# Optimization experiments

Hardware: AMD Instinct MI355X
Metric: run time of the kernel (lower is better)

The kernel has to match this reference:

```python
import jax, jax.numpy as jnp
import numpy as np

DIM = 1024
MLP_MULT = 4
NUM_EXPERTS = 8
EXPERT_HIDDEN = MLP_MULT * DIM // NUM_EXPERTS  # 512


def setup_inputs() -> dict:
    key = jax.random.key(0)
    k_x, k_r, k_fc, k_pj = jax.random.split(key, 4)
    x = jax.random.normal(k_x, (4, 4096, DIM), dtype=jnp.float32)
    # router: nn.Linear(dim, num_experts, bias=False) -> weight [E, D]
    w_router = jax.random.normal(k_r, (NUM_EXPERTS, DIM), dtype=jnp.float32) * (1.0 / np.sqrt(DIM))
    # per-expert fc: Linear(dim, hidden) weight [H, D]; stacked [E, H, D]
    w_fc = jax.random.normal(k_fc, (NUM_EXPERTS, EXPERT_HIDDEN, DIM), dtype=jnp.float32) * (1.0 / np.sqrt(DIM))
    # per-expert proj: Linear(hidden, dim) weight [D, H]; stacked [E, D, H]
    # (_zero_init in the original; use small random values so the reference output is non-trivial)
    w_proj = jax.random.normal(k_pj, (NUM_EXPERTS, DIM, EXPERT_HIDDEN), dtype=jnp.float32) * (1.0 / np.sqrt(EXPERT_HIDDEN))
    return {"x": x, "w_router": w_router, "w_fc": w_fc, "w_proj": w_proj}


def reference(x, w_router, w_fc, w_proj):
    # Router on detached input; top-1 expert per token.
    logits = jnp.einsum('bsd,ed->bse', jax.lax.stop_gradient(x), w_router)
    weights = jax.nn.softmax(logits, axis=-1)  # computed as in original (unused in output)
    indices = jnp.argmax(weights, axis=-1)     # [B, S]
    onehot = jax.nn.one_hot(indices, NUM_EXPERTS, dtype=x.dtype)  # [B, S, E]
    # Dense dispatch: run all experts, combine with one-hot (equivalent to mask gather/scatter).
    h = jnp.einsum('bsd,ehd->bseh', x, w_fc)              # [B, S, E, H]
    h = jnp.where(h >= 0, h, 0.5 * h)                      # leaky_relu(negative_slope=0.5)
    h = h * h                                              # square
    out = jnp.einsum('bseh,edh,bse->bsd', h, w_proj, onehot)
    return out
```

## Files before the change

kernel.cpp:

```cpp
#include <hip/hip_runtime.h>
#include <stdint.h>
#include <stddef.h>

#define DIM 1024
#define NEXP 8
#define HID 512
#define NTOK 16384
#define NB_HIST 64
#define NB_ROUTER 1024
#define NB_CAST 512

typedef __attribute__((ext_vector_type(4))) float f32x4;
typedef __attribute__((ext_vector_type(8))) short short8;
typedef __attribute__((ext_vector_type(4))) unsigned short u16x4;
typedef __attribute__((ext_vector_type(8))) unsigned short u16x8;
typedef __attribute__((ext_vector_type(2))) unsigned int u32x2;
typedef __attribute__((ext_vector_type(4))) unsigned int u32x4;

__device__ __forceinline__ unsigned short f2b(float f) {
  unsigned int u = __float_as_uint(f);
  return (unsigned short)((u + 0x7FFFu + ((u >> 16) & 1u)) >> 16);
}

__device__ __forceinline__ unsigned int pk_bf16(float a, float b) {
  unsigned int r;
  asm volatile("v_cvt_pk_bf16_f32 %0, %1, %2" : "=v"(r) : "v"(a), "v"(b));
  return r;
}

__device__ __forceinline__ void gload_lds16(const unsigned short* g, unsigned short* l) {
  __builtin_amdgcn_global_load_lds((const __attribute__((address_space(1))) void*)g,
                                   (__attribute__((address_space(3))) void*)l, 16, 0, 0);
}

__global__ __launch_bounds__(256) void k_router_cast(
    const float* __restrict__ x, const float* __restrict__ wr,
    int* __restrict__ eid,
    const float* __restrict__ wfc, const float* __restrict__ wpj,
    unsigned short* __restrict__ oa, unsigned short* __restrict__ ob) {
  int bid = blockIdx.x;
  if (bid < NB_ROUTER) {
    int w = threadIdx.x >> 6, lane = threadIdx.x & 63;
    int t0 = bid * 16 + w * 4;
    const float* xr = x + (size_t)t0 * DIM;
    float s[4][NEXP];
#pragma unroll
    for (int j = 0; j < 4; j++)
#pragma unroll
      for (int e = 0; e < NEXP; e++) s[j][e] = 0.f;
#pragma unroll
    for (int i = 0; i < 4; i++) {
      f32x4 xv[4];
#pragma unroll
      for (int j = 0; j < 4; j++) xv[j] = *(const f32x4*)(xr + j * DIM + lane * 4 + 256 * i);
#pragma unroll
      for (int e = 0; e < NEXP; e++) {
        f32x4 wv = *(const f32x4*)(wr + e * DIM + lane * 4 + 256 * i);
#pragma unroll
        for (int j = 0; j < 4; j++)
          s[j][e] += xv[j].x * wv.x + xv[j].y * wv.y + xv[j].z * wv.z + xv[j].w * wv.w;
      }
    }
#pragma unroll
    for (int j = 0; j < 4; j++)
#pragma unroll
      for (int e = 0; e < NEXP; e++) {
        float v = s[j][e];
#pragma unroll
        for (int off = 32; off > 0; off >>= 1) v += __shfl_xor(v, off);
        s[j][e] = v;
      }
    if (lane == 0) {
#pragma unroll
      for (int j = 0; j < 4; j++) {
        int be = 0;
        float bv = s[j][0];
#pragma unroll
        for (int e = 1; e < NEXP; e++) {
          if (s[j][e] > bv) { bv = s[j][e]; be = e; }
        }
        eid[t0 + j] = be;
      }
    }
  } else {
    const int n4 = NEXP * HID * DIM / 4;
    int stride = NB_CAST * 256;
    for (int i = (bid - NB_ROUTER) * 256 + (int)threadIdx.x; i < n4; i += stride) {
      f32x4 va = ((const f32x4*)wfc)[i];
      f32x4 vb = ((const f32x4*)wpj)[i];
      u32x2 ua, ub;
      ua.x = pk_bf16(va.x, va.y); ua.y = pk_bf16(va.z, va.w);
      ub.x = pk_bf16(vb.x, vb.y); ub.y = pk_bf16(vb.z, vb.w);
      ((u32x2*)oa)[i] = ua;
      ((u32x2*)ob)[i] = ub;
    }
  }
}

__global__ __launch_bounds__(256) void k_hist(const int* __restrict__ eid,
                                              int* __restrict__ bc) {
  __shared__ int h[NEXP];
  if (threadIdx.x < NEXP) h[threadIdx.x] = 0;
  __syncthreads();
  int tok = blockIdx.x * (NTOK / NB_HIST) + threadIdx.x;
  atomicAdd(&h[eid[tok]], 1);
  __syncthreads();
  if (threadIdx.x < NEXP) bc[blockIdx.x * NEXP + threadIdx.x] = h[threadIdx.x];
}

__global__ void k_scan(const int* __restrict__ bc, int* __restrict__ offs,
                       int* __restrict__ base) {
  __shared__ int cnt[NEXP];
  __shared__ int so[NEXP + 1];
  int t = threadIdx.x;
  if (t < NEXP) {
    int run = 0;
    for (int b = 0; b < NB_HIST; b++) {
      base[b * NEXP + t] = run;
      run += bc[b * NEXP + t];
    }
    cnt[t] = run;
  }
  __syncthreads();
  if (t == 0) {
    int a = 0;
    for (int e = 0; e < NEXP; e++) { so[e] = a; a += cnt[e]; }
    so[NEXP] = a;
  }
  __syncthreads();
  if (t < NEXP + 1) offs[t] = so[t];
  for (int i = t; i < NB_HIST * NEXP; i += blockDim.x) base[i] += so[i % NEXP];
}

__global__ __launch_bounds__(256) void k_scatter(const int* __restrict__ eid,
                                                 const int* __restrict__ base,
                                                 int* __restrict__ tlist) {
  __shared__ int cur[NEXP];
  if (threadIdx.x < NEXP) cur[threadIdx.x] = base[blockIdx.x * NEXP + threadIdx.x];
  __syncthreads();
  int tok = blockIdx.x * (NTOK / NB_HIST) + threadIdx.x;
  int e = eid[tok];
  int pos = atomicAdd(&cur[e], 1);
  tlist[pos] = tok;
}

__device__ __forceinline__ bool tile_map(const int* offs, int NB, int& e, int& mb,
                                         int& nb) {
  int l = ((int)blockIdx.x & 7) * ((int)gridDim.x >> 3) + ((int)blockIdx.x >> 3);
  e = -1; mb = 0; nb = 0;
  int acc2 = 0;
#pragma unroll
  for (int i = 0; i < NEXP; i++) {
    int mi = offs[i + 1] - offs[i];
    int tb = ((mi + 127) >> 7) * NB;
    if (e < 0 && l < acc2 + tb) {
      int r = l - acc2;
      e = i; mb = r / NB; nb = r % NB;
    }
    acc2 += tb;
  }
  return e >= 0;
}

__global__ __launch_bounds__(256) void k_gemm_fc(
    const float* __restrict__ x, const unsigned short* __restrict__ wb,
    const int* __restrict__ offs, const int* __restrict__ tlist,
    unsigned short* __restrict__ hout) {
  constexpr int KDIM = DIM, NDIM = HID;
  int e, mb, nb;
  if (!tile_map(offs, 4, e, mb, nb)) return;
  int off = offs[e], me = offs[e + 1] - off, m0 = mb * 128, n0 = nb * 128;

  __shared__ unsigned short As[3][128 * 32];
  __shared__ unsigned short Bs[3][128 * 32];

  int t = threadIdx.x, lane = t & 63, w = t >> 6;
  int wm = w >> 1, wn = w & 1;

  int kb = (lane & 3) ^ ((lane >> 3) & 3);

  const unsigned short* bsrc[2];
  const float* af32[2];
#pragma unroll
  for (int i = 0; i < 2; i++) {
    int r = i * 64 + w * 16 + (lane >> 2);
    bsrc[i] = wb + ((size_t)e * NDIM + n0 + r) * (size_t)KDIM + kb * 8;
    int gm = m0 + r;
    if (gm > me - 1) gm = me - 1;
    af32[i] = x + (size_t)tlist[off + gm] * DIM + kb * 8;
  }
  int awoff0 = (w * 16) * 32 + lane * 8;
  int awoff1 = (64 + w * 16) * 32 + lane * 8;

  f32x4 acc[4][4] = {};
  constexpr int NT = KDIM / 32;

  unsigned short* a0 = &As[0][0]; unsigned short* b0 = &Bs[0][0];
  unsigned short* a1 = &As[1][0]; unsigned short* b1 = &Bs[1][0];
  unsigned short* a2 = &As[2][0]; unsigned short* b2 = &Bs[2][0];

  f32x4 r00, r01, r10, r11;

#define ISSUE_A(kt_)                                              \
  do {                                                            \
    r00 = *(const f32x4*)(af32[0] + (kt_) * 32);                  \
    r01 = *(const f32x4*)(af32[0] + (kt_) * 32 + 4);              \
    r10 = *(const f32x4*)(af32[1] + (kt_) * 32);                  \
    r11 = *(const f32x4*)(af32[1] + (kt_) * 32 + 4);              \
  } while (0)
#define ISSUE_B(kt_, db_)                                         \
  do {                                                            \
    gload_lds16(bsrc[0] + (kt_) * 32, (db_) + (w * 16) * 32);     \
    gload_lds16(bsrc[1] + (kt_) * 32, (db_) + (64 + w * 16) * 32);\
  } while (0)
#define WRITE_A(da_)                                              \
  do {                                                            \
    u32x4 c0, c1;                                                 \
    c0.x = pk_bf16(r00.x, r00.y); c0.y = pk_bf16(r00.z, r00.w);   \
    c0.z = pk_bf16(r01.x, r01.y); c0.w = pk_bf16(r01.z, r01.w);   \
    c1.x = pk_bf16(r10.x, r10.y); c1.y = pk_bf16(r10.z, r10.w);   \
    c1.z = pk_bf16(r11.x, r11.y); c1.w = pk_bf16(r11.z, r11.w);   \
    *(u32x4*)&(da_)[awoff0] = c0;                                 \
    *(u32x4*)&(da_)[awoff1] = c1;                                 \
  } while (0)

  ISSUE_A(0);
  ISSUE_B(0, b0);
  ISSUE_B(1, b1);

  for (int kt = 0; kt < NT; kt++) {
    if (kt == NT - 1) {
      asm volatile("s_waitcnt vmcnt(0)" ::: "memory");
    } else {
      asm volatile("s_waitcnt vmcnt(2)" ::: "memory");
    }
    __builtin_amdgcn_sched_barrier(0);
    WRITE_A(a0);
    asm volatile("s_waitcnt lgkmcnt(0)" ::: "memory");
    __builtin_amdgcn_sched_barrier(0);
    __builtin_amdgcn_s_barrier();
    if (kt + 1 < NT) ISSUE_A(kt + 1);
    if (kt + 2 < NT) ISSUE_B(kt + 2, b2);

    short8 af[4], bf[4];
#pragma unroll
    for (int i = 0; i < 4; i++) {
      int ra = wm * 64 + i * 16 + (lane & 15);
      int ca = (lane >> 4) ^ ((ra >> 1) & 3);
      af[i] = *(const short8*)&a0[ra * 32 + ca * 8];
      int rbb = wn * 64 + i * 16 + (lane & 15);
      int cb = (lane >> 4) ^ ((rbb >> 1) & 3);
      bf[i] = *(const short8*)&b0[rbb * 32 + cb * 8];
    }
    __builtin_amdgcn_s_setprio(1);
#pragma unroll
    for (int mi = 0; mi < 4; mi++)
#pragma unroll
      for (int ni = 0; ni < 4; ni++)
        acc[mi][ni] =
            __builtin_amdgcn_mfma_f32_16x16x32_bf16(af[mi], bf[ni], acc[mi][ni], 0, 0, 0);
    __builtin_amdgcn_s_setprio(0);

    unsigned short* ta = a0; a0 = a1; a1 = a2; a2 = ta;
    unsigned short* tb = b0; b0 = b1; b1 = b2; b2 = tb;
  }
#undef ISSUE_A
#undef ISSUE_B
#undef WRITE_A

  int rb = (lane >> 4) * 4, cb = lane & 15;
#pragma unroll
  for (int mi = 0; mi < 4; mi++) {
#pragma unroll
    for (int j = 0; j < 4; j++) {
      int ml = wm * 64 + mi * 16 + rb + j;
      if (m0 + ml < me) {
#pragma unroll
        for (int ni = 0; ni < 4; ni++) {
          int col = n0 + wn * 64 + ni * 16 + cb;
          float v = acc[mi][ni][j];
          v = (v >= 0.f) ? v * v : 0.25f * v * v;
          hout[(size_t)(off + m0 + ml) * HID + col] = f2b(v);
        }
      }
    }
  }
}

__global__ __launch_bounds__(256) void k_gemm_pj(
    const unsigned short* __restrict__ hin, const unsigned short* __restrict__ wb,
    const int* __restrict__ offs, const int* __restrict__ tlist,
    float* __restrict__ out) {
  constexpr int KDIM = HID, NDIM = DIM;
  int e, mb, nb;
  if (!tile_map(offs, 8, e, mb, nb)) return;
  int off = offs[e], me = offs[e + 1] - off, m0 = mb * 128, n0 = nb * 128;

  __shared__ unsigned short lds[3][2][128 * 32];

  int t = threadIdx.x, lane = t & 63, w = t >> 6;
  int wm = w >> 1, wn = w & 1;

  int kb = (lane & 3) ^ ((lane >> 3) & 3);

  const unsigned short* asrc[2];
  const unsigned short* bsrc[2];
#pragma unroll
  for (int i = 0; i < 2; i++) {
    int r = i * 64 + w * 16 + (lane >> 2);
    int gm = m0 + r;
    if (gm > me - 1) gm = me - 1;
    asrc[i] = hin + (size_t)(off + gm) * KDIM + kb * 8;
    bsrc[i] = wb + ((size_t)e * NDIM + n0 + r) * (size_t)KDIM + kb * 8;
  }

  f32x4 acc[4][4] = {};
  constexpr int NT = KDIM / 32;

  unsigned short* b0a = &lds[0][0][0]; unsigned short* b0b = &lds[0][1][0];
  unsigned short* b1a = &lds[1][0][0]; unsigned short* b1b = &lds[1][1][0];
  unsigned short* b2a = &lds[2][0][0]; unsigned short* b2b = &lds[2][1][0];

#define STAGE(kt_, da_, db_)                                       \
  do {                                                             \
    gload_lds16(asrc[0] + (kt_) * 32, (da_) + (w * 16) * 32);      \
    gload_lds16(asrc[1] + (kt_) * 32, (da_) + (64 + w * 16) * 32); \
    gload_lds16(bsrc[0] + (kt_) * 32, (db_) + (w * 16) * 32);      \
    gload_lds16(bsrc[1] + (kt_) * 32, (db_) + (64 + w * 16) * 32); \
  } while (0)

  STAGE(0, b0a, b0b);
  STAGE(1, b1a, b1b);

  for (int kt = 0; kt < NT; kt++) {
    if (kt < NT - 1) {
      asm volatile("s_waitcnt vmcnt(4)" ::: "memory");
    } else {
      asm volatile("s_waitcnt vmcnt(0)" ::: "memory");
    }
    __builtin_amdgcn_s_barrier();

    if (kt + 2 < NT) STAGE(kt + 2, b2a, b2b);

    short8 af[4], bf[4];
#pragma unroll
    for (int i = 0; i < 4; i++) {
      int ra = wm * 64 + i * 16 + (lane & 15);
      int ca = (lane >> 4) ^ ((ra >> 1) & 3);
      af[i] = *(const short8*)&b0a[ra * 32 + ca * 8];
      int rbb = wn * 64 + i * 16 + (lane & 15);
      int cb = (lane >> 4) ^ ((rbb >> 1) & 3);
      bf[i] = *(const short8*)&b0b[rbb * 32 + cb * 8];
    }
    __builtin_amdgcn_s_setprio(1);
#pragma unroll
    for (int mi = 0; mi < 4; mi++)
#pragma unroll
      for (int ni = 0; ni < 4; ni++)
        acc[mi][ni] =
            __builtin_amdgcn_mfma_f32_16x16x32_bf16(af[mi], bf[ni], acc[mi][ni], 0, 0, 0);
    __builtin_amdgcn_s_setprio(0);

    unsigned short* ta = b0a; b0a = b1a; b1a = b2a; b2a = ta;
    unsigned short* tb = b0b; b0b = b1b; b1b = b2b; b2b = tb;
  }
#undef STAGE

  int rb = (lane >> 4) * 4, cb = lane & 15;
#pragma unroll
  for (int mi = 0; mi < 4; mi++) {
#pragma unroll
    for (int j = 0; j < 4; j++) {
      int ml = wm * 64 + mi * 16 + rb + j;
      if (m0 + ml < me) {
        int tok = tlist[off + m0 + ml];
#pragma unroll
        for (int ni = 0; ni < 4; ni++) {
          int col = n0 + wn * 64 + ni * 16 + cb;
          out[(size_t)tok * DIM + col] = acc[mi][ni][j];
        }
      }
    }
  }
}

extern "C" void kernel_launch(void* const* d_in, const int* in_sizes, int n_in,
                              void* d_out, int out_size, void* d_ws, size_t ws_size,
                              hipStream_t stream) {
  const float* x = (const float*)d_in[0];
  const float* wr = (const float*)d_in[1];
  const float* wfc = (const float*)d_in[2];
  const float* wpj = (const float*)d_in[3];
  float* out = (float*)d_out;

  uintptr_t p = (uintptr_t)d_ws;
  int* offs = (int*)p;  p += 256;
  int* bc = (int*)p;    p += sizeof(int) * NB_HIST * NEXP;
  int* base = (int*)p;  p += sizeof(int) * NB_HIST * NEXP;
  int* eid = (int*)p;   p += sizeof(int) * NTOK;
  int* tlist = (int*)p; p += sizeof(int) * NTOK;
  unsigned short* wfc_b = (unsigned short*)p; p += (size_t)NEXP * HID * DIM * 2;
  unsigned short* wpj_b = (unsigned short*)p; p += (size_t)NEXP * DIM * HID * 2;
  unsigned short* hbuf = (unsigned short*)p;  p += (size_t)NTOK * HID * 2;

  k_router_cast<<<NB_ROUTER + NB_CAST, 256, 0, stream>>>(
      x, wr, eid, wfc, wpj, wfc_b, wpj_b);
  k_hist<<<NB_HIST, 256, 0, stream>>>(eid, bc);
  k_scan<<<1, 256, 0, stream>>>(bc, offs, base);
  k_scatter<<<NB_HIST, 256, 0, stream>>>(eid, base, tlist);
  k_gemm_fc<<<dim3(544), 256, 0, stream>>>(x, wfc_b, offs, tlist, hbuf);
  k_gemm_pj<<<dim3(1080), 256, 0, stream>>>(hbuf, wpj_b, offs, tlist, out);
}
```

Before: 104.8 us.

## Move proj-weight bf16 cast into fc GEMM launch to overlap with compute

The fp32-to-bf16 cast of the projection weights moves out of the router/cast kernel into extra leading blocks of the fc GEMM launch. The cast's memory traffic can then overlap with the compute-bound fc GEMM tiles instead of lengthening the memory-bound router kernel. The tile mapping is generalized to take an explicit block offset and grid size. The cast blocks occupy CUs at the start of the fc launch and may delay some GEMM tiles.

```diff
diff --git a/kernel.cpp b/kernel.cpp
--- a/kernel.cpp
+++ b/kernel.cpp
@@ -9,6 +9,8 @@
 #define NB_HIST 64
 #define NB_ROUTER 1024
 #define NB_CAST 512
+#define NB_CAST_PJ 256
+#define NB_FC_TILES 544
 
 typedef __attribute__((ext_vector_type(4))) float f32x4;
 typedef __attribute__((ext_vector_type(8))) short short8;
@@ -36,8 +38,7 @@
 __global__ __launch_bounds__(256) void k_router_cast(
     const float* __restrict__ x, const float* __restrict__ wr,
     int* __restrict__ eid,
-    const float* __restrict__ wfc, const float* __restrict__ wpj,
-    unsigned short* __restrict__ oa, unsigned short* __restrict__ ob) {
+    const float* __restrict__ wfc, unsigned short* __restrict__ oa) {
   int bid = blockIdx.x;
   if (bid < NB_ROUTER) {
     int w = threadIdx.x >> 6, lane = threadIdx.x & 63;
@@ -87,12 +88,9 @@
     int stride = NB_CAST * 256;
     for (int i = (bid - NB_ROUTER) * 256 + (int)threadIdx.x; i < n4; i += stride) {
       f32x4 va = ((const f32x4*)wfc)[i];
-      f32x4 vb = ((const f32x4*)wpj)[i];
-      u32x2 ua, ub;
+      u32x2 ua;
       ua.x = pk_bf16(va.x, va.y); ua.y = pk_bf16(va.z, va.w);
-      ub.x = pk_bf16(vb.x, vb.y); ub.y = pk_bf16(vb.z, vb.w);
       ((u32x2*)oa)[i] = ua;
-      ((u32x2*)ob)[i] = ub;
     }
   }
 }
@@ -144,9 +142,9 @@
   tlist[pos] = tok;
 }
 
-__device__ __forceinline__ bool tile_map(const int* offs, int NB, int& e, int& mb,
-                                         int& nb) {
-  int l = ((int)blockIdx.x & 7) * ((int)gridDim.x >> 3) + ((int)blockIdx.x >> 3);
+__device__ __forceinline__ bool tile_map_g(const int* offs, int NB, int bid, int G,
+                                           int& e, int& mb, int& nb) {
+  int l = (bid & 7) * (G >> 3) + (bid >> 3);
   e = -1; mb = 0; nb = 0;
   int acc2 = 0;
 #pragma unroll
@@ -165,10 +163,22 @@
 __global__ __launch_bounds__(256) void k_gemm_fc(
     const float* __restrict__ x, const unsigned short* __restrict__ wb,
     const int* __restrict__ offs, const int* __restrict__ tlist,
-    unsigned short* __restrict__ hout) {
+    unsigned short* __restrict__ hout,
+    const float* __restrict__ wpj, unsigned short* __restrict__ wpj_b) {
+  if (blockIdx.x < NB_CAST_PJ) {
+    const int n4 = NEXP * DIM * HID / 4;
+    int stride = NB_CAST_PJ * 256;
+    for (int i = blockIdx.x * 256 + (int)threadIdx.x; i < n4; i += stride) {
+      f32x4 vb = ((const f32x4*)wpj)[i];
+      u32x2 ub;
+      ub.x = pk_bf16(vb.x, vb.y); ub.y = pk_bf16(vb.z, vb.w);
+      ((u32x2*)wpj_b)[i] = ub;
+    }
+    return;
+  }
   constexpr int KDIM = DIM, NDIM = HID;
   int e, mb, nb;
-  if (!tile_map(offs, 4, e, mb, nb)) return;
+  if (!tile_map_g(offs, 4, (int)blockIdx.x - NB_CAST_PJ, NB_FC_TILES, e, mb, nb)) return;
   int off = offs[e], me = offs[e + 1] - off, m0 = mb * 128, n0 = nb * 128;
 
   __shared__ unsigned short As[3][128 * 32];
@@ -293,7 +303,7 @@
     float* __restrict__ out) {
   constexpr int KDIM = HID, NDIM = DIM;
   int e, mb, nb;
-  if (!tile_map(offs, 8, e, mb, nb)) return;
+  if (!tile_map_g(offs, 8, (int)blockIdx.x, (int)gridDim.x, e, mb, nb)) return;
   int off = offs[e], me = offs[e + 1] - off, m0 = mb * 128, n0 = nb * 128;
 
   __shared__ unsigned short lds[3][2][128 * 32];
@@ -403,11 +413,11 @@
   unsigned short* wpj_b = (unsigned short*)p; p += (size_t)NEXP * DIM * HID * 2;
   unsigned short* hbuf = (unsigned short*)p;  p += (size_t)NTOK * HID * 2;
 
-  k_router_cast<<<NB_ROUTER + NB_CAST, 256, 0, stream>>>(
-      x, wr, eid, wfc, wpj, wfc_b, wpj_b);
+  k_router_cast<<<NB_ROUTER + NB_CAST, 256, 0, stream>>>(x, wr, eid, wfc, wfc_b);
   k_hist<<<NB_HIST, 256, 0, stream>>>(eid, bc);
   k_scan<<<1, 256, 0, stream>>>(bc, offs, base);
   k_scatter<<<NB_HIST, 256, 0, stream>>>(eid, base, tlist);
-  k_gemm_fc<<<dim3(544), 256, 0, stream>>>(x, wfc_b, offs, tlist, hbuf);
+  k_gemm_fc<<<dim3(NB_CAST_PJ + NB_FC_TILES), 256, 0, stream>>>(
+      x, wfc_b, offs, tlist, hbuf, wpj, wpj_b);
   k_gemm_pj<<<dim3(1080), 256, 0, stream>>>(hbuf, wpj_b, offs, tlist, out);
 }
```

Result: no change. 105.5 us (+0.7%).

## Stage fp32 activations directly to LDS via async loads, convert at fragment read

Applied to the files above, without the earlier changes.

The fc GEMM now loads the gathered fp32 x rows straight into LDS with global_load_lds, using a swizzled fp32 layout. It no longer goes through registers, converting to bf16 and writing to LDS. The bf16 pack moves to the point where MFMA fragments are read from LDS. This removes the register round trip and the lgkm wait before the barrier, so A and B share one async pipeline. In exchange the A buffers use twice the LDS (fp32), which may lower occupancy, and each tile reread repeats the conversion work.

```diff
diff --git a/kernel.cpp b/kernel.cpp
--- a/kernel.cpp
+++ b/kernel.cpp
@@ -12,8 +12,6 @@
 
 typedef __attribute__((ext_vector_type(4))) float f32x4;
 typedef __attribute__((ext_vector_type(8))) short short8;
-typedef __attribute__((ext_vector_type(4))) unsigned short u16x4;
-typedef __attribute__((ext_vector_type(8))) unsigned short u16x8;
 typedef __attribute__((ext_vector_type(2))) unsigned int u32x2;
 typedef __attribute__((ext_vector_type(4))) unsigned int u32x4;
 
@@ -28,7 +26,7 @@
   return r;
 }
 
-__device__ __forceinline__ void gload_lds16(const unsigned short* g, unsigned short* l) {
+__device__ __forceinline__ void gload_lds16(const void* g, void* l) {
   __builtin_amdgcn_global_load_lds((const __attribute__((address_space(1))) void*)g,
                                    (__attribute__((address_space(3))) void*)l, 16, 0, 0);
 }
@@ -144,9 +142,9 @@
   tlist[pos] = tok;
 }
 
-__device__ __forceinline__ bool tile_map(const int* offs, int NB, int& e, int& mb,
-                                         int& nb) {
-  int l = ((int)blockIdx.x & 7) * ((int)gridDim.x >> 3) + ((int)blockIdx.x >> 3);
+__device__ __forceinline__ bool tile_map_g(const int* offs, int NB, int bid, int G,
+                                           int& e, int& mb, int& nb) {
+  int l = (bid & 7) * (G >> 3) + (bid >> 3);
   e = -1; mb = 0; nb = 0;
   int acc2 = 0;
 #pragma unroll
@@ -168,86 +166,75 @@
     unsigned short* __restrict__ hout) {
   constexpr int KDIM = DIM, NDIM = HID;
   int e, mb, nb;
-  if (!tile_map(offs, 4, e, mb, nb)) return;
+  if (!tile_map_g(offs, 4, (int)blockIdx.x, (int)gridDim.x, e, mb, nb)) return;
   int off = offs[e], me = offs[e + 1] - off, m0 = mb * 128, n0 = nb * 128;
 
-  __shared__ unsigned short As[3][128 * 32];
+  __shared__ float Af[3][128 * 32];
   __shared__ unsigned short Bs[3][128 * 32];
 
   int t = threadIdx.x, lane = t & 63, w = t >> 6;
   int wm = w >> 1, wn = w & 1;
 
+  int cha = ((lane & 7) ^ ((lane >> 3) & 7)) * 4;
   int kb = (lane & 3) ^ ((lane >> 3) & 3);
 
+  const float* asrcf[4];
+#pragma unroll
+  for (int i = 0; i < 4; i++) {
+    int r = i * 32 + w * 8 + (lane >> 3);
+    int gm = m0 + r;
+    if (gm > me - 1) gm = me - 1;
+    asrcf[i] = x + (size_t)tlist[off + gm] * DIM + cha;
+  }
   const unsigned short* bsrc[2];
-  const float* af32[2];
 #pragma unroll
   for (int i = 0; i < 2; i++) {
     int r = i * 64 + w * 16 + (lane >> 2);
     bsrc[i] = wb + ((size_t)e * NDIM + n0 + r) * (size_t)KDIM + kb * 8;
-    int gm = m0 + r;
-    if (gm > me - 1) gm = me - 1;
-    af32[i] = x + (size_t)tlist[off + gm] * DIM + kb * 8;
-  }
-  int awoff0 = (w * 16) * 32 + lane * 8;
-  int awoff1 = (64 + w * 16) * 32 + lane * 8;
+  }
 
   f32x4 acc[4][4] = {};
   constexpr int NT = KDIM / 32;
 
-  unsigned short* a0 = &As[0][0]; unsigned short* b0 = &Bs[0][0];
-  unsigned short* a1 = &As[1][0]; unsigned short* b1 = &Bs[1][0];
-  unsigned short* a2 = &As[2][0]; unsigned short* b2 = &Bs[2][0];
-
-  f32x4 r00, r01, r10, r11;
-
-#define ISSUE_A(kt_)                                              \
-  do {                                                            \
-    r00 = *(const f32x4*)(af32[0] + (kt_) * 32);                  \
-    r01 = *(const f32x4*)(af32[0] + (kt_) * 32 + 4);              \
-    r10 = *(const f32x4*)(af32[1] + (kt_) * 32);                  \
-    r11 = *(const f32x4*)(af32[1] + (kt_) * 32 + 4);              \
+  float* a0 = &Af[0][0]; unsigned short* b0 = &Bs[0][0];
+  float* a1 = &Af[1][0]; unsigned short* b1 = &Bs[1][0];
+  float* a2 = &Af[2][0]; unsigned short* b2 = &Bs[2][0];
+
+#define STAGE(kt_, da_, db_)                                           \
+  do {                                                                 \
+    gload_lds16(asrcf[0] + (kt_) * 32, (da_) + (0 * 32 + w * 8) * 32); \
+    gload_lds16(asrcf[1] + (kt_) * 32, (da_) + (1 * 32 + w * 8) * 32); \
+    gload_lds16(asrcf[2] + (kt_) * 32, (da_) + (2 * 32 + w * 8) * 32); \
+    gload_lds16(asrcf[3] + (kt_) * 32, (da_) + (3 * 32 + w * 8) * 32); \
+    gload_lds16(bsrc[0] + (kt_) * 32, (db_) + (w * 16) * 32);          \
+    gload_lds16(bsrc[1] + (kt_) * 32, (db_) + (64 + w * 16) * 32);     \
   } while (0)
-#define ISSUE_B(kt_, db_)                                         \
-  do {                                                            \
-    gload_lds16(bsrc[0] + (kt_) * 32, (db_) + (w * 16) * 32);     \
-    gload_lds16(bsrc[1] + (kt_) * 32, (db_) + (64 + w * 16) * 32);\
-  } while (0)
-#define WRITE_A(da_)                                              \
-  do {                                                            \
-    u32x4 c0, c1;                                                 \
-    c0.x = pk_bf16(r00.x, r00.y); c0.y = pk_bf16(r00.z, r00.w);   \
-    c0.z = pk_bf16(r01.x, r01.y); c0.w = pk_bf16(r01.z, r01.w);   \
-    c1.x = pk_bf16(r10.x, r10.y); c1.y = pk_bf16(r10.z, r10.w);   \
-    c1.z = pk_bf16(r11.x, r11.y); c1.w = pk_bf16(r11.z, r11.w);   \
-    *(u32x4*)&(da_)[awoff0] = c0;                                 \
-    *(u32x4*)&(da_)[awoff1] = c1;                                 \
-  } while (0)
-
-  ISSUE_A(0);
-  ISSUE_B(0, b0);
-  ISSUE_B(1, b1);
+
+  STAGE(0, a0, b0);
+  STAGE(1, a1, b1);
 
   for (int kt = 0; kt < NT; kt++) {
-    if (kt == NT - 1) {
+    if (kt < NT - 1) {
+      asm volatile("s_waitcnt vmcnt(6)" ::: "memory");
+    } else {
       asm volatile("s_waitcnt vmcnt(0)" ::: "memory");
-    } else {
-      asm volatile("s_waitcnt vmcnt(2)" ::: "memory");
-    }
-    __builtin_amdgcn_sched_barrier(0);
-    WRITE_A(a0);
-    asm volatile("s_waitcnt lgkmcnt(0)" ::: "memory");
-    __builtin_amdgcn_sched_barrier(0);
+    }
     __builtin_amdgcn_s_barrier();
-    if (kt + 1 < NT) ISSUE_A(kt + 1);
-    if (kt + 2 < NT) ISSUE_B(kt + 2, b2);
+
+    if (kt + 2 < NT) STAGE(kt + 2, a2, b2);
 
     short8 af[4], bf[4];
 #pragma unroll
     for (int i = 0; i < 4; i++) {
       int ra = wm * 64 + i * 16 + (lane & 15);
-      int ca = (lane >> 4) ^ ((ra >> 1) & 3);
-      af[i] = *(const short8*)&a0[ra * 32 + ca * 8];
+      int c = lane >> 4;
+      int s0 = (2 * c) ^ (ra & 7), s1 = (2 * c + 1) ^ (ra & 7);
+      f32x4 lo = *(const f32x4*)&a0[ra * 32 + s0 * 4];
+      f32x4 hi = *(const f32x4*)&a0[ra * 32 + s1 * 4];
+      u32x4 pkv;
+      pkv.x = pk_bf16(lo.x, lo.y); pkv.y = pk_bf16(lo.z, lo.w);
+      pkv.z = pk_bf16(hi.x, hi.y); pkv.w = pk_bf16(hi.z, hi.w);
+      af[i] = *(short8*)&pkv;
       int rbb = wn * 64 + i * 16 + (lane & 15);
       int cb = (lane >> 4) ^ ((rbb >> 1) & 3);
       bf[i] = *(const short8*)&b0[rbb * 32 + cb * 8];
@@ -261,12 +248,10 @@
             __builtin_amdgcn_mfma_f32_16x16x32_bf16(af[mi], bf[ni], acc[mi][ni], 0, 0, 0);
     __builtin_amdgcn_s_setprio(0);
 
-    unsigned short* ta = a0; a0 = a1; a1 = a2; a2 = ta;
+    float* ta = a0; a0 = a1; a1 = a2; a2 = ta;
     unsigned short* tb = b0; b0 = b1; b1 = b2; b2 = tb;
   }
-#undef ISSUE_A
-#undef ISSUE_B
-#undef WRITE_A
+#undef STAGE
 
   int rb = (lane >> 4) * 4, cb = lane & 15;
 #pragma unroll
@@ -293,7 +278,7 @@
     float* __restrict__ out) {
   constexpr int KDIM = HID, NDIM = DIM;
   int e, mb, nb;
-  if (!tile_map(offs, 8, e, mb, nb)) return;
+  if (!tile_map_g(offs, 8, (int)blockIdx.x, (int)gridDim.x, e, mb, nb)) return;
   int off = offs[e], me = offs[e + 1] - off, m0 = mb * 128, n0 = nb * 128;
 
   __shared__ unsigned short lds[3][2][128 * 32];
```

After: 136.0 us. +29.8%, slower.
